# Optimization experiments

Hardware: AMD Instinct MI355X
Metric: run time of the kernel (lower is better)

## Reference

```python
import jax, jax.numpy as jnp
import numpy as np

NUM_USERS = 1_000_000
NUM_MOVIES = 100_000
NUM_GENRES = 32
EDIM = 64
GMF_DIM = EDIM + EDIM // 2  # 96
BATCH = 65536
GENRES_PER_MOVIE = 3


def setup_inputs() -> dict:
    key = jax.random.key(0)
    ks = jax.random.split(key, 16)
    std = 0.01
    inp = {
        "user_ids": jax.random.randint(ks[0], (BATCH,), 0, NUM_USERS, dtype=jnp.int32),
        "movie_ids": jax.random.randint(ks[1], (BATCH,), 0, NUM_MOVIES, dtype=jnp.int32),
        "genre_ids": jax.random.randint(ks[2], (BATCH * GENRES_PER_MOVIE,), 0, NUM_GENRES, dtype=jnp.int32),
        "offsets": (jnp.arange(BATCH, dtype=jnp.int32) * GENRES_PER_MOVIE),
        "user_mem_w": jax.random.normal(ks[3], (NUM_USERS, 1)) * std,
        "movie_mem_w": jax.random.normal(ks[4], (NUM_MOVIES, 1)) * std,
        "ue_gmf": jax.random.normal(ks[5], (NUM_USERS, GMF_DIM)) * std,
        "me_gmf": jax.random.normal(ks[6], (NUM_MOVIES, EDIM)) * std,
        "ge_gmf": jax.random.normal(ks[7], (NUM_GENRES, EDIM // 2)) * std,
        "ue_mlp": jax.random.normal(ks[8], (NUM_USERS, GMF_DIM)) * std,
        "me_mlp": jax.random.normal(ks[9], (NUM_MOVIES, EDIM)) * std,
        "ge_mlp": jax.random.normal(ks[10], (NUM_GENRES, EDIM // 2)) * std,
        # mlp_layer: Linear(192,64) -> ReLU -> Linear(64,96) -> ReLU (torch [out,in] convention)
        "w1": jax.random.normal(ks[11], (64, EDIM * 3)) * (1.0 / np.sqrt(EDIM * 3)),
        "b1": jnp.zeros((64,)),
        "w2": jax.random.normal(ks[12], (GMF_DIM, 64)) * (1.0 / np.sqrt(64)),
        "b2": jnp.zeros((GMF_DIM,)),
        "w_out": jax.random.normal(ks[13], (1, EDIM * 3)) * (1.0 / np.sqrt(EDIM * 3)),
        "b_out": jnp.zeros((1,)),
    }
    return inp


def _bag_mean(table, ids, offsets, num_bags):
    # EmbeddingBag(mode='mean') with flat ids + offsets
    total = ids.shape[0]
    emb = table[ids]  # [total, d]
    seg = jnp.searchsorted(offsets, jnp.arange(total, dtype=offsets.dtype), side="right") - 1
    sums = jax.ops.segment_sum(emb, seg, num_segments=num_bags)
    counts = jnp.diff(jnp.concatenate([offsets, jnp.array([total], dtype=offsets.dtype)]))
    return sums / jnp.maximum(counts, 1).astype(sums.dtype)[:, None]


def reference(user_ids, movie_ids, genre_ids, offsets,
              user_mem_w, movie_mem_w,
              ue_gmf, me_gmf, ge_gmf,
              ue_mlp, me_mlp, ge_mlp,
              w1, b1, w2, b2, w_out, b_out):
    B = user_ids.shape[0]
    user_mem = user_mem_w[user_ids]    # [B,1]
    movie_mem = movie_mem_w[movie_ids]  # [B,1]

    user_g = ue_gmf[user_ids]  # [B,96]
    movie_g = jnp.concatenate([me_gmf[movie_ids], _bag_mean(ge_gmf, genre_ids, offsets, B)], axis=1)  # [B,96]
    gmf_out = user_g * movie_g  # [B,96]

    user_m = ue_mlp[user_ids]
    movie_m = jnp.concatenate([me_mlp[movie_ids], _bag_mean(ge_mlp, genre_ids, offsets, B)], axis=1)
    h = jnp.concatenate([user_m, movie_m], axis=1)  # [B,192]
    h = jax.nn.relu(h @ w1.T + b1)
    mlp_out = jax.nn.relu(h @ w2.T + b2)  # [B,96]

    cat = jnp.concatenate([gmf_out, mlp_out], axis=1)  # [B,192]
    out = cat @ w_out.T + b_out  # [B,1]
    return (user_mem + movie_mem + out).squeeze(-1)  # [B]
```

## Files before the change

kernel.cpp:

```cpp
#include <hip/hip_runtime.h>

#define BT 64
#define NTHREADS 256

typedef __attribute__((ext_vector_type(8))) __bf16 bf16x8;
typedef __attribute__((ext_vector_type(4))) __bf16 bf16x4;
typedef __attribute__((ext_vector_type(4))) float f32x4;

__device__ __forceinline__ __bf16 f2bf(float f) { return (__bf16)f; }
__device__ __forceinline__ f32x4 ld4(const float* p) { return *(const f32x4*)p; }

__global__ __launch_bounds__(NTHREADS, 4)
void ncf_one(const int* __restrict__ user_ids, const int* __restrict__ movie_ids,
             const int* __restrict__ genre_ids, const int* __restrict__ offsets,
             const float* __restrict__ user_mem_w, const float* __restrict__ movie_mem_w,
             const float* __restrict__ ue_gmf, const float* __restrict__ me_gmf,
             const float* __restrict__ ge_gmf,
             const float* __restrict__ ue_mlp, const float* __restrict__ me_mlp,
             const float* __restrict__ ge_mlp,
             const float* __restrict__ w1, const float* __restrict__ b1,
             const float* __restrict__ w2, const float* __restrict__ b2,
             const float* __restrict__ w_out, const float* __restrict__ b_out,
             float* __restrict__ out, int Btot, int totG)
{
    __shared__ __bf16 SA[64 * 200];
    __shared__ __bf16 WL2[96 * 72];

    const int tid  = threadIdx.x;
    const int lane = tid & 63;
    const int wid  = tid >> 6;
    const int lr   = lane & 15;
    const int lg   = lane >> 4;
    const int e0   = blockIdx.x * BT;

    #pragma unroll
    for (int j = 0; j < 12; ++j) {
        const int v = tid + j * 256;
        const int r = v / 48, c4 = v % 48;
        f32x4 a = ld4(w1 + (size_t)v * 4);
        bf16x4 t; t[0]=f2bf(a[0]); t[1]=f2bf(a[1]); t[2]=f2bf(a[2]); t[3]=f2bf(a[3]);
        *(bf16x4*)&SA[r * 200 + c4 * 4] = t;
    }
    #pragma unroll
    for (int j = 0; j < 6; ++j) {
        const int v = tid + j * 256;
        const int r = v >> 4, c4 = v & 15;
        f32x4 a = ld4(w2 + (size_t)v * 4);
        bf16x4 t; t[0]=f2bf(a[0]); t[1]=f2bf(a[1]); t[2]=f2bf(a[2]); t[3]=f2bf(a[3]);
        *(bf16x4*)&WL2[r * 72 + c4 * 4] = t;
    }

    const int erow = wid * 16 + lr;
    const int gidx = min(e0 + erow, Btot - 1);
    const int u    = user_ids[gidx];
    const int mv   = movie_ids[gidx];
    const int gs   = offsets[gidx];
    const int gend = (gidx + 1 < Btot) ? offsets[gidx + 1] : totG;
    const int cnt  = gend - gs;
    const float inv = 1.0f / (float)(cnt > 0 ? cnt : 1);

    f32x4 gg0 = {0.f,0.f,0.f,0.f}, gg1 = {0.f,0.f,0.f,0.f};
    f32x4 gm0 = {0.f,0.f,0.f,0.f}, gm1 = {0.f,0.f,0.f,0.f};
    for (int i = gs; i < gend; ++i) {
        const int g = genre_ids[i];
        const float* pg = ge_gmf + (size_t)g * 32 + 4 * lg;
        gg0 += ld4(pg);
        gg1 += ld4(pg + 16);
        const float* pm = ge_mlp + (size_t)g * 32 + 8 * lg;
        gm0 += ld4(pm);
        gm1 += ld4(pm + 4);
    }

    bf16x8 fr[6];
    {
        const float* up = ue_mlp + (size_t)u * 96 + lg * 8;
        const float* mp = me_mlp + (size_t)mv * 64 + lg * 8;
        #pragma unroll
        for (int kt = 0; kt < 3; ++kt) {
            f32x4 a = ld4(up + kt * 32), b = ld4(up + kt * 32 + 4);
            bf16x8 t;
            t[0]=f2bf(a[0]); t[1]=f2bf(a[1]); t[2]=f2bf(a[2]); t[3]=f2bf(a[3]);
            t[4]=f2bf(b[0]); t[5]=f2bf(b[1]); t[6]=f2bf(b[2]); t[7]=f2bf(b[3]);
            fr[kt] = t;
        }
        #pragma unroll
        for (int kt = 0; kt < 2; ++kt) {
            f32x4 a = ld4(mp + kt * 32), b = ld4(mp + kt * 32 + 4);
            bf16x8 t;
            t[0]=f2bf(a[0]); t[1]=f2bf(a[1]); t[2]=f2bf(a[2]); t[3]=f2bf(a[3]);
            t[4]=f2bf(b[0]); t[5]=f2bf(b[1]); t[6]=f2bf(b[2]); t[7]=f2bf(b[3]);
            fr[3 + kt] = t;
        }
        bf16x8 t;
        t[0]=f2bf(gm0[0]*inv); t[1]=f2bf(gm0[1]*inv); t[2]=f2bf(gm0[2]*inv); t[3]=f2bf(gm0[3]*inv);
        t[4]=f2bf(gm1[0]*inv); t[5]=f2bf(gm1[1]*inv); t[6]=f2bf(gm1[2]*inv); t[7]=f2bf(gm1[3]*inv);
        fr[5] = t;
    }

    float pval;
    {
        float s = 0.f;
        #pragma unroll
        for (int j = 0; j < 4; ++j) {
            const int d = 4 * lg + 16 * j;
            f32x4 ug = ld4(ue_gmf + (size_t)u * 96 + d);
            f32x4 mg = ld4(me_gmf + (size_t)mv * 64 + d);
            f32x4 wo = ld4(w_out + d);
            s += ug[0]*mg[0]*wo[0] + ug[1]*mg[1]*wo[1] + ug[2]*mg[2]*wo[2] + ug[3]*mg[3]*wo[3];
        }
        {
            const int d = 64 + 4 * lg;
            f32x4 ug = ld4(ue_gmf + (size_t)u * 96 + d);
            f32x4 wo = ld4(w_out + d);
            s += ug[0]*gg0[0]*inv*wo[0] + ug[1]*gg0[1]*inv*wo[1]
               + ug[2]*gg0[2]*inv*wo[2] + ug[3]*gg0[3]*inv*wo[3];
        }
        {
            const int d = 80 + 4 * lg;
            f32x4 ug = ld4(ue_gmf + (size_t)u * 96 + d);
            f32x4 wo = ld4(w_out + d);
            s += ug[0]*gg1[0]*inv*wo[0] + ug[1]*gg1[1]*inv*wo[1]
               + ug[2]*gg1[2]*inv*wo[2] + ug[3]*gg1[3]*inv*wo[3];
        }
        if (lg == 0) s += user_mem_w[u] + movie_mem_w[mv] + b_out[0];
        s += __shfl_xor(s, 16);
        s += __shfl_xor(s, 32);
        pval = s;
    }

    __syncthreads();

    f32x4 acc1[4] = {};
    #pragma unroll
    for (int kt = 0; kt < 6; ++kt) {
        #pragma unroll
        for (int nt = 0; nt < 4; ++nt) {
            bf16x8 bw = *(const bf16x8*)&SA[(nt * 16 + lr) * 200 + kt * 32 + lg * 8];
            acc1[nt] = __builtin_amdgcn_mfma_f32_16x16x32_bf16(fr[kt], bw, acc1[nt], 0, 0, 0);
        }
    }

    __syncthreads();

    #pragma unroll
    for (int nt = 0; nt < 4; ++nt) {
        const float bv = b1[nt * 16 + lr];
        #pragma unroll
        for (int r = 0; r < 4; ++r) {
            float v = acc1[nt][r] + bv;
            v = v > 0.f ? v : 0.f;
            SA[(wid * 16 + lg * 4 + r) * 72 + nt * 16 + lr] = f2bf(v);
        }
    }
    __syncthreads();

    f32x4 acc2[6] = {};
    #pragma unroll
    for (int kt = 0; kt < 2; ++kt) {
        bf16x8 av = *(const bf16x8*)&SA[(wid * 16 + lr) * 72 + kt * 32 + lg * 8];
        #pragma unroll
        for (int nt = 0; nt < 6; ++nt) {
            bf16x8 bw = *(const bf16x8*)&WL2[(nt * 16 + lr) * 72 + kt * 32 + lg * 8];
            acc2[nt] = __builtin_amdgcn_mfma_f32_16x16x32_bf16(av, bw, acc2[nt], 0, 0, 0);
        }
    }

    float s0 = 0.f, s1 = 0.f, s2 = 0.f, s3 = 0.f;
    #pragma unroll
    for (int nt = 0; nt < 6; ++nt) {
        const int col = nt * 16 + lr;
        const float b2v = b2[col];
        const float wo  = w_out[96 + col];
        float v;
        v = acc2[nt][0] + b2v; v = v > 0.f ? v : 0.f; s0 += v * wo;
        v = acc2[nt][1] + b2v; v = v > 0.f ? v : 0.f; s1 += v * wo;
        v = acc2[nt][2] + b2v; v = v > 0.f ? v : 0.f; s2 += v * wo;
        v = acc2[nt][3] + b2v; v = v > 0.f ? v : 0.f; s3 += v * wo;
    }
    #pragma unroll
    for (int mask = 1; mask <= 8; mask <<= 1) {
        s0 += __shfl_xor(s0, mask);
        s1 += __shfl_xor(s1, mask);
        s2 += __shfl_xor(s2, mask);
        s3 += __shfl_xor(s3, mask);
    }
    const float p0 = __shfl(pval, lg * 4 + 0);
    const float p1 = __shfl(pval, lg * 4 + 1);
    const float p2 = __shfl(pval, lg * 4 + 2);
    const float p3 = __shfl(pval, lg * 4 + 3);

    if (lr == 0) {
        const int rowb = e0 + wid * 16 + lg * 4;
        if (rowb + 0 < Btot) out[rowb + 0] = p0 + s0;
        if (rowb + 1 < Btot) out[rowb + 1] = p1 + s1;
        if (rowb + 2 < Btot) out[rowb + 2] = p2 + s2;
        if (rowb + 3 < Btot) out[rowb + 3] = p3 + s3;
    }
}

extern "C" void kernel_launch(void* const* d_in, const int* in_sizes, int n_in,
                              void* d_out, int out_size, void* d_ws, size_t ws_size,
                              hipStream_t stream) {
    const int*   user_ids    = (const int*)d_in[0];
    const int*   movie_ids   = (const int*)d_in[1];
    const int*   genre_ids   = (const int*)d_in[2];
    const int*   offsets     = (const int*)d_in[3];
    const float* user_mem_w  = (const float*)d_in[4];
    const float* movie_mem_w = (const float*)d_in[5];
    const float* ue_gmf      = (const float*)d_in[6];
    const float* me_gmf      = (const float*)d_in[7];
    const float* ge_gmf      = (const float*)d_in[8];
    const float* ue_mlp      = (const float*)d_in[9];
    const float* me_mlp      = (const float*)d_in[10];
    const float* ge_mlp      = (const float*)d_in[11];
    const float* w1          = (const float*)d_in[12];
    const float* b1          = (const float*)d_in[13];
    const float* w2          = (const float*)d_in[14];
    const float* b2          = (const float*)d_in[15];
    const float* w_out       = (const float*)d_in[16];
    const float* b_out       = (const float*)d_in[17];

    const int Btot = in_sizes[0];
    const int totG = in_sizes[2];

    const int grid = (Btot + BT - 1) / BT;
    ncf_one<<<grid, NTHREADS, 0, stream>>>(
        user_ids, movie_ids, genre_ids, offsets,
        user_mem_w, movie_mem_w,
        ue_gmf, me_gmf, ge_gmf,
        ue_mlp, me_mlp, ge_mlp,
        w1, b1, w2, b2, w_out, b_out,
        (float*)d_out, Btot, totG);
}
```

Baseline: 28.18 us.

## Double rows per block and hoist all embedding gathers ahead of weight staging

Raises the block tile from 64 to 128 rows (512 threads), so each block's w1/w2 bf16 staging into shared memory is spread over twice as many rows and each thread does half as many staging loads. All per-row gathers (ue_mlp, me_mlp, ue_gmf, me_gmf, user/movie memory weights) are now issued up front, before the genre loop and the weight staging, so more independent memory requests are in flight at once. In exchange, more values stay live in registers, which under the unchanged launch bounds risks spills or lower occupancy. The larger block also depends on the unseen code and shared buffers handling 128 rows correctly.

```diff
diff --git a/kernel.cpp b/kernel.cpp
--- a/kernel.cpp
+++ b/kernel.cpp
@@ -1,7 +1,7 @@
 #include <hip/hip_runtime.h>
 
-#define BT 64
-#define NTHREADS 256
+#define BT 128
+#define NTHREADS 512
 
 typedef __attribute__((ext_vector_type(8))) __bf16 bf16x8;
 typedef __attribute__((ext_vector_type(4))) __bf16 bf16x4;
@@ -33,23 +33,6 @@
     const int lg   = lane >> 4;
     const int e0   = blockIdx.x * BT;
 
-    #pragma unroll
-    for (int j = 0; j < 12; ++j) {
-        const int v = tid + j * 256;
-        const int r = v / 48, c4 = v % 48;
-        f32x4 a = ld4(w1 + (size_t)v * 4);
-        bf16x4 t; t[0]=f2bf(a[0]); t[1]=f2bf(a[1]); t[2]=f2bf(a[2]); t[3]=f2bf(a[3]);
-        *(bf16x4*)&SA[r * 200 + c4 * 4] = t;
-    }
-    #pragma unroll
-    for (int j = 0; j < 6; ++j) {
-        const int v = tid + j * 256;
-        const int r = v >> 4, c4 = v & 15;
-        f32x4 a = ld4(w2 + (size_t)v * 4);
-        bf16x4 t; t[0]=f2bf(a[0]); t[1]=f2bf(a[1]); t[2]=f2bf(a[2]); t[3]=f2bf(a[3]);
-        *(bf16x4*)&WL2[r * 72 + c4 * 4] = t;
-    }
-
     const int erow = wid * 16 + lr;
     const int gidx = min(e0 + erow, Btot - 1);
     const int u    = user_ids[gidx];
@@ -58,6 +41,22 @@
     const int gend = (gidx + 1 < Btot) ? offsets[gidx + 1] : totG;
     const int cnt  = gend - gs;
     const float inv = 1.0f / (float)(cnt > 0 ? cnt : 1);
+
+    const float* up = ue_mlp + (size_t)u * 96 + lg * 8;
+    const float* mp = me_mlp + (size_t)mv * 64 + lg * 8;
+    f32x4 ua0 = ld4(up +  0), ub0 = ld4(up +  4),
+          ua1 = ld4(up + 32), ub1 = ld4(up + 36),
+          ua2 = ld4(up + 64), ub2 = ld4(up + 68);
+    f32x4 ma0 = ld4(mp +  0), mb0 = ld4(mp +  4),
+          ma1 = ld4(mp + 32), mb1 = ld4(mp + 36);
+
+    const float* ugp = ue_gmf + (size_t)u * 96 + 4 * lg;
+    f32x4 ug0 = ld4(ugp +  0), ug1 = ld4(ugp + 16), ug2 = ld4(ugp + 32),
+          ug3 = ld4(ugp + 48), ug4 = ld4(ugp + 64), ug5 = ld4(ugp + 80);
+    const float* mgp = me_gmf + (size_t)mv * 64 + 4 * lg;
+    f32x4 mg0 = ld4(mgp + 0), mg1 = ld4(mgp + 16), mg2 = ld4(mgp + 32), mg3 = ld4(mgp + 48);
+    const float um = user_mem_w[u];
+    const float mm = movie_mem_w[mv];
 
     f32x4 gg0 = {0.f,0.f,0.f,0.f}, gg1 = {0.f,0.f,0.f,0.f};
     f32x4 gm0 = {0.f,0.f,0.f,0.f}, gm1 = {0.f,0.f,0.f,0.f};
@@ -71,27 +70,41 @@
         gm1 += ld4(pm + 4);
     }
 
+    #pragma unroll
+    for (int j = 0; j < 6; ++j) {
+        const int v = tid + j * 512;
+        const int r = v / 48, c4 = v % 48;
+        f32x4 a = ld4(w1 + (size_t)v * 4);
+        bf16x4 t; t[0]=f2bf(a[0]); t[1]=f2bf(a[1]); t[2]=f2bf(a[2]); t[3]=f2bf(a[3]);
+        *(bf16x4*)&SA[r * 200 + c4 * 4] = t;
+    }
+    #pragma unroll
+    for (int j = 0; j < 3; ++j) {
+        const int v = tid + j * 512;
+        const int r = v >> 4, c4 = v & 15;
+        f32x4 a = ld4(w2 + (size_t)v * 4);
+        bf16x4 t; t[0]=f2bf(a[0]); t[1]=f2bf(a[1]); t[2]=f2bf(a[2]); t[3]=f2bf(a[3]);
+        *(bf16x4*)&WL2[r * 72 + c4 * 4] = t;
+    }
+
     bf16x8 fr[6];
     {
-        const float* up = ue_mlp + (size_t)u * 96 + lg * 8;
-        const float* mp = me_mlp + (size_t)mv * 64 + lg * 8;
-        #pragma unroll
-        for (int kt = 0; kt < 3; ++kt) {
-            f32x4 a = ld4(up + kt * 32), b = ld4(up + kt * 32 + 4);
-            bf16x8 t;
-            t[0]=f2bf(a[0]); t[1]=f2bf(a[1]); t[2]=f2bf(a[2]); t[3]=f2bf(a[3]);
-            t[4]=f2bf(b[0]); t[5]=f2bf(b[1]); t[6]=f2bf(b[2]); t[7]=f2bf(b[3]);
-            fr[kt] = t;
-        }
-        #pragma unroll
-        for (int kt = 0; kt < 2; ++kt) {
-            f32x4 a = ld4(mp + kt * 32), b = ld4(mp + kt * 32 + 4);
-            bf16x8 t;
-            t[0]=f2bf(a[0]); t[1]=f2bf(a[1]); t[2]=f2bf(a[2]); t[3]=f2bf(a[3]);
-            t[4]=f2bf(b[0]); t[5]=f2bf(b[1]); t[6]=f2bf(b[2]); t[7]=f2bf(b[3]);
-            fr[3 + kt] = t;
-        }
         bf16x8 t;
+        t[0]=f2bf(ua0[0]); t[1]=f2bf(ua0[1]); t[2]=f2bf(ua0[2]); t[3]=f2bf(ua0[3]);
+        t[4]=f2bf(ub0[0]); t[5]=f2bf(ub0[1]); t[6]=f2bf(ub0[2]); t[7]=f2bf(ub0[3]);
+        fr[0] = t;
+        t[0]=f2bf(ua1[0]); t[1]=f2bf(ua1[1]); t[2]=f2bf(ua1[2]); t[3]=f2bf(ua1[3]);
+        t[4]=f2bf(ub1[0]); t[5]=f2bf(ub1[1]); t[6]=f2bf(ub1[2]); t[7]=f2bf(ub1[3]);
+        fr[1] = t;
+        t[0]=f2bf(ua2[0]); t[1]=f2bf(ua2[1]); t[2]=f2bf(ua2[2]); t[3]=f2bf(ua2[3]);
+        t[4]=f2bf(ub2[0]); t[5]=f2bf(ub2[1]); t[6]=f2bf(ub2[2]); t[7]=f2bf(ub2[3]);
+        fr[2] = t;
+        t[0]=f2bf(ma0[0]); t[1]=f2bf(ma0[1]); t[2]=f2bf(ma0[2]); t[3]=f2bf(ma0[3]);
+        t[4]=f2bf(mb0[0]); t[5]=f2bf(mb0[1]); t[6]=f2bf(mb0[2]); t[7]=f2bf(mb0[3]);
+        fr[3] = t;
+        t[0]=f2bf(ma1[0]); t[1]=f2bf(ma1[1]); t[2]=f2bf(ma1[2]); t[3]=f2bf(ma1[3]);
+        t[4]=f2bf(mb1[0]); t[5]=f2bf(mb1[1]); t[6]=f2bf(mb1[2]); t[7]=f2bf(mb1[3]);
+        fr[4] = t;
         t[0]=f2bf(gm0[0]*inv); t[1]=f2bf(gm0[1]*inv); t[2]=f2bf(gm0[2]*inv); t[3]=f2bf(gm0[3]*inv);
         t[4]=f2bf(gm1[0]*inv); t[5]=f2bf(gm1[1]*inv); t[6]=f2bf(gm1[2]*inv); t[7]=f2bf(gm1[3]*inv);
         fr[5] = t;
@@ -99,30 +112,17 @@
 
     float pval;
     {
+        const float* wop = w_out + 4 * lg;
+        f32x4 wo0 = ld4(wop), wo1 = ld4(wop + 16), wo2 = ld4(wop + 32),
+              wo3 = ld4(wop + 48), wo4 = ld4(wop + 64), wo5 = ld4(wop + 80);
         float s = 0.f;
         #pragma unroll
-        for (int j = 0; j < 4; ++j) {
-            const int d = 4 * lg + 16 * j;
-            f32x4 ug = ld4(ue_gmf + (size_t)u * 96 + d);
-            f32x4 mg = ld4(me_gmf + (size_t)mv * 64 + d);
-            f32x4 wo = ld4(w_out + d);
-            s += ug[0]*mg[0]*wo[0] + ug[1]*mg[1]*wo[1] + ug[2]*mg[2]*wo[2] + ug[3]*mg[3]*wo[3];
-        }
-        {
-            const int d = 64 + 4 * lg;
-            f32x4 ug = ld4(ue_gmf + (size_t)u * 96 + d);
-            f32x4 wo = ld4(w_out + d);
-            s += ug[0]*gg0[0]*inv*wo[0] + ug[1]*gg0[1]*inv*wo[1]
-               + ug[2]*gg0[2]*inv*wo[2] + ug[3]*gg0[3]*inv*wo[3];
-        }
-        {
-            const int d = 80 + 4 * lg;
-            f32x4 ug = ld4(ue_gmf + (size_t)u * 96 + d);
-            f32x4 wo = ld4(w_out + d);
-            s += ug[0]*gg1[0]*inv*wo[0] + ug[1]*gg1[1]*inv*wo[1]
-               + ug[2]*gg1[2]*inv*wo[2] + ug[3]*gg1[3]*inv*wo[3];
-        }
-        if (lg == 0) s += user_mem_w[u] + movie_mem_w[mv] + b_out[0];
+        for (int q = 0; q < 4; ++q) {
+            s += ug0[q]*mg0[q]*wo0[q] + ug1[q]*mg1[q]*wo1[q]
+               + ug2[q]*mg2[q]*wo2[q] + ug3[q]*mg3[q]*wo3[q];
+            s += ug4[q]*(gg0[q]*inv)*wo4[q] + ug5[q]*(gg1[q]*inv)*wo5[q];
+        }
+        if (lg == 0) s += um + mm + b_out[0];
         s += __shfl_xor(s, 16);
         s += __shfl_xor(s, 32);
         pval = s;
```

After: 34.76 us. 1.23x slower.
